# Performance work log

Hardware: AMD Instinct MI355X
Metric: run time of the kernel (lower is better)

Reference implementation:

```python
import jax, jax.numpy as jnp
import numpy as np

IOU_THRESH = 0.6
IMG_SIZE = 2048.0


def _iou_matrix(boxes):
    # boxes: [N, 4] as (x1, y1, x2, y2)
    x1, y1, x2, y2 = boxes[:, 0], boxes[:, 1], boxes[:, 2], boxes[:, 3]
    area = jnp.maximum(x2 - x1, 0.0) * jnp.maximum(y2 - y1, 0.0)  # [N]
    ix1 = jnp.maximum(x1[:, None], x1[None, :])
    iy1 = jnp.maximum(y1[:, None], y1[None, :])
    ix2 = jnp.minimum(x2[:, None], x2[None, :])
    iy2 = jnp.minimum(y2[:, None], y2[None, :])
    inter = jnp.maximum(ix2 - ix1, 0.0) * jnp.maximum(iy2 - iy1, 0.0)  # [N, N]
    union = area[:, None] + area[None, :] - inter
    return inter / jnp.maximum(union, 1e-9)


def _nms_keep(boxes, thresh):
    # Greedy NMS in the given (score-sorted) order; returns a [N] bool keep mask.
    n = boxes.shape[0]
    iou = _iou_matrix(boxes)  # [N, N] -- dominant memory traffic
    idx = jnp.arange(n)

    def step(suppressed, i):
        keep_i = jnp.logical_not(suppressed[i])
        # a kept box suppresses all LATER boxes with IoU > thresh
        suppressed = suppressed | (keep_i & (idx > i) & (iou[i] > thresh))
        return suppressed, keep_i

    _, keep = jax.lax.scan(step, jnp.zeros((n,), dtype=bool), idx)
    return keep


def _make_boxes(kc, ks, n):
    c = jax.random.uniform(kc, (n, 2), minval=0.0, maxval=IMG_SIZE)
    s = jax.random.uniform(ks, (n, 2), minval=10.0, maxval=120.0)
    return jnp.concatenate([c - s / 2, c + s / 2], axis=1)  # [n, 4]


def setup_inputs() -> dict:
    key = jax.random.key(0)
    k1, k2, k3, k4, k5, k6 = jax.random.split(key, 6)
    N = 8192  # vstacked detections across projections
    M = 8192  # vstacked RPN rois across projections
    det_boxes = _make_boxes(k1, k2, N)
    cls_scores = jax.random.normal(k3, (N, 4), dtype=jnp.float32)  # 4 TL classes, class 0 = invalid
    proj_id = jnp.zeros((N, 1), dtype=jnp.float32)
    detections = jnp.concatenate([proj_id, det_boxes, cls_scores], axis=1)  # [N, 9]
    rpn_boxes = _make_boxes(k4, k5, M)
    objness = jax.random.uniform(k6, (M, 1), dtype=jnp.float32)
    rpn_data = jnp.concatenate([jnp.zeros((M, 1), dtype=jnp.float32), rpn_boxes, objness], axis=1)  # [M, 6]
    return {"detections": detections, "rpn_data": rpn_data}


def reference(detections, rpn_data):
    # detect(): NMS(0.6) on detections[:, 1:5] and on rpn_data[:, 1:5]
    keep_det = _nms_keep(detections[:, 1:5], IOU_THRESH)  # [N] bool
    keep_rpn = _nms_keep(rpn_data[:, 1:5], IOU_THRESH)    # [M] bool
    # forward(): split surviving detections into valid (tl_type != 0) / invalid
    tl_types = jnp.argmax(detections[:, 5:], axis=1)
    valid_mask = keep_det & (tl_types != 0)
    invalid_mask = keep_det & (tl_types == 0)
    # fixed-shape (jit-friendly) masked outputs instead of data-dependent gather
    valid_detections = detections * valid_mask[:, None].astype(detections.dtype)
    invalid_detections = detections * invalid_mask[:, None].astype(detections.dtype)
    rpn_attack_data = rpn_data * keep_rpn[:, None].astype(rpn_data.dtype)
    return valid_detections, invalid_detections, rpn_attack_data
```

## Files before the change

### kernel.cpp

```cpp
#include <hip/hip_runtime.h>


constexpr int NROWS = 8192;
constexpr int NKW   = 256;
constexpr unsigned BCAP = 1536;
constexpr unsigned ACAP = 512;
constexpr unsigned RCAP = 2048;
constexpr unsigned ELDS = 16384;
#define IOU_T 0.6f

constexpr size_t OFF_EDGES = 4096;

__global__ __launch_bounds__(512) void scanpair_kernel(
    const float* __restrict__ det, const float* __restrict__ rpn,
    unsigned* __restrict__ cnts, unsigned* __restrict__ edges)
{
  const int cellid = blockIdx.x, set = blockIdx.y;
  const float* src  = (set == 0) ? det : rpn;
  const int    strd = (set == 0) ? 9 : 6;
  unsigned* myedges = edges + ((size_t)(set * 256 + cellid)) * RCAP;
  const int cx = cellid & 15, cy = cellid >> 4;

  __shared__ float Bx1[BCAP], By1[BCAP], Bx2[BCAP], By2[BCAP], Bar[BCAP];
  __shared__ unsigned Bid[BCAP];
  __shared__ unsigned aList[ACAP];
  __shared__ unsigned bCnt, aCnt, eCnt, ovf;

  const int t = threadIdx.x;
  if (t == 0) { bCnt = 0u; aCnt = 0u; eCnt = 0u; ovf = 0u; }
  __syncthreads();

  #pragma unroll
  for (int base = 0; base < 16; base += 8) {
    float rx1[8], ry1[8], rx2[8], ry2[8];
    #pragma unroll
    for (int k = 0; k < 8; ++k) {
      const int r = t + (base + k) * 512;
      const float* p = src + (size_t)r * strd + 1;
      rx1[k] = p[0]; ry1[k] = p[1]; rx2[k] = p[2]; ry2[k] = p[3];
    }
    #pragma unroll
    for (int k = 0; k < 8; ++k) {
      const int r = t + (base + k) * 512;
      const float x1 = rx1[k], y1 = ry1[k], x2 = rx2[k], y2 = ry2[k];
      const float cxe = 0.5f * (x1 + x2), cye = 0.5f * (y1 + y2);
      const int ccx = min(15, max(0, (int)(cxe * (1.0f / 128.0f))));
      const int ccy = min(15, max(0, (int)(cye * (1.0f / 128.0f))));
      const int dx = ccx - cx, dy = ccy - cy;
      if (dx >= -1 && dx <= 1 && dy >= -1 && dy <= 1) {
        const unsigned s = atomicAdd(&bCnt, 1u);
        if (s < BCAP) {
          Bx1[s] = x1; By1[s] = y1; Bx2[s] = x2; By2[s] = y2;
          Bar[s] = fmaxf(x2 - x1, 0.0f) * fmaxf(y2 - y1, 0.0f);
          Bid[s] = (unsigned)r;
          if (dx == 0 && dy == 0) {
            const unsigned as = atomicAdd(&aCnt, 1u);
            if (as < ACAP) aList[as] = s; else atomicOr(&ovf, 1u);
          }
        } else atomicOr(&ovf, 1u);
      }
    }
  }
  __syncthreads();

  const unsigned nb = min(bCnt, BCAP);
  const unsigned na = min(aCnt, ACAP);

  if (!ovf) {
    const unsigned tot = na * nb;
    for (unsigned p = t; p < tot; p += 512) {
      const unsigned ai = p / nb, x = p - ai * nb;
      const unsigned s = aList[ai];
      const unsigned ia = Bid[s], ib = Bid[x];
      if (ia < ib) {
        const float ix1 = fmaxf(Bx1[s], Bx1[x]), iy1 = fmaxf(By1[s], By1[x]);
        const float ix2 = fminf(Bx2[s], Bx2[x]), iy2 = fminf(By2[s], By2[x]);
        const float inter = fmaxf(ix2 - ix1, 0.0f) * fmaxf(iy2 - iy1, 0.0f);
        if (inter > 0.0f) {
          const float uni = Bar[s] + Bar[x] - inter;
          const float iou = inter / fmaxf(uni, 1e-9f);
          if (iou > IOU_T) {
            const unsigned slot = atomicAdd(&eCnt, 1u);
            if (slot < RCAP) myedges[slot] = (ia << 13) | ib;
          }
        }
      }
    }
  } else {
    for (int ra = 0; ra < NROWS; ++ra) {
      const float* pa = src + (size_t)ra * strd + 1;
      const float ax1 = pa[0], ay1 = pa[1], ax2 = pa[2], ay2 = pa[3];
      const float cxe = 0.5f * (ax1 + ax2), cye = 0.5f * (ay1 + ay2);
      const int ccx = min(15, max(0, (int)(cxe * (1.0f / 128.0f))));
      const int ccy = min(15, max(0, (int)(cye * (1.0f / 128.0f))));
      if (ccx != cx || ccy != cy) continue;
      const float aar = fmaxf(ax2 - ax1, 0.0f) * fmaxf(ay2 - ay1, 0.0f);
      for (int rb = t; rb < NROWS; rb += 512) {
        if ((unsigned)ra >= (unsigned)rb) continue;
        const float* pb = src + (size_t)rb * strd + 1;
        const float bx1 = pb[0], by1 = pb[1], bx2 = pb[2], by2 = pb[3];
        const float ix1 = fmaxf(ax1, bx1), iy1 = fmaxf(ay1, by1);
        const float ix2 = fminf(ax2, bx2), iy2 = fminf(ay2, by2);
        const float inter = fmaxf(ix2 - ix1, 0.0f) * fmaxf(iy2 - iy1, 0.0f);
        if (inter > 0.0f) {
          const float bar = fmaxf(bx2 - bx1, 0.0f) * fmaxf(by2 - by1, 0.0f);
          const float uni = aar + bar - inter;
          const float iou = inter / fmaxf(uni, 1e-9f);
          if (iou > IOU_T) {
            const unsigned slot = atomicAdd(&eCnt, 1u);
            if (slot < RCAP) myedges[slot] = ((unsigned)ra << 13) | (unsigned)rb;
          }
        }
      }
    }
  }
  __syncthreads();
  if (t == 0) cnts[set * 256 + cellid] = min(eCnt, RCAP);
}

__global__ __launch_bounds__(1024) void solve_epi_kernel(
    const float* __restrict__ det, const float* __restrict__ rpn,
    const unsigned* __restrict__ cnts, const unsigned* __restrict__ edges,
    float* __restrict__ out)
{
  const int blk = blockIdx.x;
  const int set = blk >> 4;
  const int slice = blk & 15;
  const unsigned* gedges = edges + (size_t)set * 256 * RCAP;

  __shared__ unsigned eL[ELDS];
  __shared__ unsigned rcnt[256], roff[256];
  __shared__ unsigned kbuf[2][NKW];
  __shared__ int changed[2];
  __shared__ unsigned Etot_sh;

  const int t = threadIdx.x;
  if (t < 256) rcnt[t] = min(cnts[set * 256 + t], RCAP);
  __syncthreads();

  if (t < 64) {
    const unsigned h0 = rcnt[4 * t], h1 = rcnt[4 * t + 1];
    const unsigned h2 = rcnt[4 * t + 2], h3 = rcnt[4 * t + 3];
    const unsigned lsum = h0 + h1 + h2 + h3;
    unsigned incl = lsum;
    #pragma unroll
    for (int d = 1; d < 64; d <<= 1) {
      const unsigned v = __shfl_up(incl, d);
      if (t >= d) incl += v;
    }
    const unsigned base = incl - lsum;
    roff[4 * t] = base;               roff[4 * t + 1] = base + h0;
    roff[4 * t + 2] = base + h0 + h1; roff[4 * t + 3] = base + h0 + h1 + h2;
    if (t == 63) Etot_sh = incl;
  }
  if (t < NKW) kbuf[0][t] = 0xFFFFFFFFu;
  __syncthreads();

  const unsigned Etot = Etot_sh;
  const bool cached = (Etot <= ELDS);
  if (cached) {
    const unsigned rg = (unsigned)t >> 2, ln = (unsigned)t & 3u;
    const unsigned c = rcnt[rg], o = roff[rg];
    for (unsigned k = ln; k < c; k += 4u)
      eL[o + k] = gedges[(size_t)rg * RCAP + k];
  }
  __syncthreads();

  int cur = 0;
  for (int round = 0; round < NROWS + 8; ++round) {
    const int nxt = cur ^ 1;
    if (t == 0) changed[round & 1] = 0;
    if (t < NKW) kbuf[nxt][t] = 0xFFFFFFFFu;
    __syncthreads();

    if (cached) {
      for (unsigned e = t; e < Etot; e += 1024) {
        const unsigned pk = eL[e];
        const unsigned i = pk >> 13, j = pk & 8191u;
        if ((kbuf[cur][i >> 5] >> (i & 31)) & 1u)
          atomicAnd(&kbuf[nxt][j >> 5], ~(1u << (j & 31)));
      }
    } else {
      for (unsigned r = (unsigned)t >> 2; r < 256u; r += 256u) {
        const unsigned c = rcnt[r];
        for (unsigned k = (unsigned)t & 3u; k < c; k += 4u) {
          const unsigned pk = gedges[(size_t)r * RCAP + k];
          const unsigned i = pk >> 13, j = pk & 8191u;
          if ((kbuf[cur][i >> 5] >> (i & 31)) & 1u)
            atomicAnd(&kbuf[nxt][j >> 5], ~(1u << (j & 31)));
        }
      }
    }
    __syncthreads();

    if (t < NKW && kbuf[nxt][t] != kbuf[cur][t]) changed[round & 1] = 1;
    __syncthreads();

    cur = nxt;
    if (!changed[round & 1]) break;
  }

  const int r0 = slice * 512;
  if (set == 0) {
    for (int i = r0 + t; i < r0 + 512; i += 1024) {
      const bool kd = (kbuf[cur][i >> 5] >> (i & 31)) & 1u;
      const float* p = det + (size_t)i * 9;
      const float sc0 = p[5], sc1 = p[6], sc2 = p[7], sc3 = p[8];
      int am = 0; float best = sc0;
      if (sc1 > best) { best = sc1; am = 1; }
      if (sc2 > best) { best = sc2; am = 2; }
      if (sc3 > best) { best = sc3; am = 3; }
      const float vm = (kd && am != 0) ? 1.0f : 0.0f;
      const float im = (kd && am == 0) ? 1.0f : 0.0f;
      float* o0 = out + (size_t)i * 9;
      float* o1 = out + (size_t)NROWS * 9 + (size_t)i * 9;
      #pragma unroll
      for (int c = 0; c < 9; ++c) { const float v = p[c]; o0[c] = v * vm; o1[c] = v * im; }
    }
  } else {
    for (int i = r0 + t; i < r0 + 512; i += 1024) {
      const bool kr = (kbuf[cur][i >> 5] >> (i & 31)) & 1u;
      const float rm = kr ? 1.0f : 0.0f;
      const float* q = rpn + (size_t)i * 6;
      float* o2 = out + (size_t)NROWS * 18 + (size_t)i * 6;
      #pragma unroll
      for (int c = 0; c < 6; ++c) o2[c] = q[c] * rm;
    }
  }
}

extern "C" void kernel_launch(void* const* d_in, const int* in_sizes, int n_in,
                              void* d_out, int out_size, void* d_ws, size_t ws_size,
                              hipStream_t stream)
{
  const float* det = (const float*)d_in[0];
  const float* rpn = (const float*)d_in[1];
  float* out = (float*)d_out;

  char* ws = (char*)d_ws;
  unsigned* cnts  = (unsigned*)ws;
  unsigned* edges = (unsigned*)(ws + OFF_EDGES);

  dim3 g1(256, 2);
  scanpair_kernel<<<g1, 512, 0, stream>>>(det, rpn, cnts, edges);
  solve_epi_kernel<<<32, 1024, 0, stream>>>(det, rpn, cnts, edges, out);
}
```

Baseline: 75.47 us.

## Replace per-cell pair blocks with per-row strip blocks using counting-sort binning

The pair-finding kernel now uses one block per grid row (16×2 blocks) instead of one per cell (256×2). Each block counting-sorts the boxes from its three neighbouring rows into column bins, then loops over the 16 cells in that row and tests each cell's boxes against its 3×3 neighbourhood. This cuts the number of blocks that each read all 8192 boxes, so far less redundant global load and binning work is done. The cost is a second input pass, a serial loop over columns inside each block, and only 32 blocks to fill the GPU. The solve kernel's edge-list bookkeeping shrinks to 16 rows per set to match.

```diff
diff --git a/kernel.cpp b/kernel.cpp
--- a/kernel.cpp
+++ b/kernel.cpp
@@ -3,33 +3,36 @@
 
 constexpr int NROWS = 8192;
 constexpr int NKW   = 256;
-constexpr unsigned BCAP = 1536;
-constexpr unsigned ACAP = 512;
-constexpr unsigned RCAP = 2048;
+constexpr unsigned SCAP = 2048;
+constexpr unsigned MCAP = 768;
+constexpr unsigned RCAP = 4096;
 constexpr unsigned ELDS = 16384;
 #define IOU_T 0.6f
 
 constexpr size_t OFF_EDGES = 4096;
 
-__global__ __launch_bounds__(512) void scanpair_kernel(
+__global__ __launch_bounds__(512) void strip_kernel(
     const float* __restrict__ det, const float* __restrict__ rpn,
     unsigned* __restrict__ cnts, unsigned* __restrict__ edges)
 {
-  const int cellid = blockIdx.x, set = blockIdx.y;
+  const int cy = blockIdx.x, set = blockIdx.y;
   const float* src  = (set == 0) ? det : rpn;
   const int    strd = (set == 0) ? 9 : 6;
-  unsigned* myedges = edges + ((size_t)(set * 256 + cellid)) * RCAP;
-  const int cx = cellid & 15, cy = cellid >> 4;
-
-  __shared__ float Bx1[BCAP], By1[BCAP], Bx2[BCAP], By2[BCAP], Bar[BCAP];
-  __shared__ unsigned Bid[BCAP];
-  __shared__ unsigned aList[ACAP];
-  __shared__ unsigned bCnt, aCnt, eCnt, ovf;
+  unsigned* myedges = edges + (size_t)(set * 16 + cy) * RCAP;
+
+  __shared__ float Sx1[SCAP], Sy1[SCAP], Sx2[SCAP], Sy2[SCAP], Sar[SCAP];
+  __shared__ unsigned Sid[SCAP];
+  __shared__ unsigned mlist[MCAP];
+  __shared__ unsigned shist[16], scur[16], soff[17];
+  __shared__ unsigned mhist[16], mcur[16], moff[17];
+  __shared__ unsigned eCnt, ovf;
 
   const int t = threadIdx.x;
-  if (t == 0) { bCnt = 0u; aCnt = 0u; eCnt = 0u; ovf = 0u; }
-  __syncthreads();
-
+  if (t < 16) { shist[t] = 0u; mhist[t] = 0u; scur[t] = 0u; mcur[t] = 0u; }
+  if (t == 0) { eCnt = 0u; ovf = 0u; }
+  __syncthreads();
+
+  int rcls[16];
   #pragma unroll
   for (int base = 0; base < 16; base += 8) {
     float rx1[8], ry1[8], rx2[8], ry2[8];
@@ -41,21 +44,59 @@
     }
     #pragma unroll
     for (int k = 0; k < 8; ++k) {
-      const int r = t + (base + k) * 512;
       const float x1 = rx1[k], y1 = ry1[k], x2 = rx2[k], y2 = ry2[k];
       const float cxe = 0.5f * (x1 + x2), cye = 0.5f * (y1 + y2);
       const int ccx = min(15, max(0, (int)(cxe * (1.0f / 128.0f))));
       const int ccy = min(15, max(0, (int)(cye * (1.0f / 128.0f))));
-      const int dx = ccx - cx, dy = ccy - cy;
-      if (dx >= -1 && dx <= 1 && dy >= -1 && dy <= 1) {
-        const unsigned s = atomicAdd(&bCnt, 1u);
-        if (s < BCAP) {
-          Bx1[s] = x1; By1[s] = y1; Bx2[s] = x2; By2[s] = y2;
-          Bar[s] = fmaxf(x2 - x1, 0.0f) * fmaxf(y2 - y1, 0.0f);
-          Bid[s] = (unsigned)r;
-          if (dx == 0 && dy == 0) {
-            const unsigned as = atomicAdd(&aCnt, 1u);
-            if (as < ACAP) aList[as] = s; else atomicOr(&ovf, 1u);
+      int cls = -1;
+      if (ccy >= cy - 1 && ccy <= cy + 1) {
+        cls = ccx | ((ccy == cy) ? 256 : 0);
+        atomicAdd(&shist[ccx], 1u);
+        if (ccy == cy) atomicAdd(&mhist[ccx], 1u);
+      }
+      rcls[base + k] = cls;
+    }
+  }
+  __syncthreads();
+
+  if (t < 64) {
+    const unsigned sv = (t < 16) ? shist[t] : 0u;
+    const unsigned mv = (t < 16) ? mhist[t] : 0u;
+    unsigned si = sv, mi = mv;
+    #pragma unroll
+    for (int d = 1; d < 16; d <<= 1) {
+      const unsigned a = __shfl_up(si, d);
+      const unsigned b = __shfl_up(mi, d);
+      if (t >= d) { si += a; mi += b; }
+    }
+    if (t < 16) { soff[t] = si - sv; moff[t] = mi - mv; }
+    if (t == 15) { soff[16] = si; moff[16] = mi; }
+  }
+  __syncthreads();
+
+  #pragma unroll
+  for (int base = 0; base < 16; base += 8) {
+    float rx1[8], ry1[8], rx2[8], ry2[8];
+    #pragma unroll
+    for (int k = 0; k < 8; ++k) {
+      const int r = t + (base + k) * 512;
+      const float* p = src + (size_t)r * strd + 1;
+      rx1[k] = p[0]; ry1[k] = p[1]; rx2[k] = p[2]; ry2[k] = p[3];
+    }
+    #pragma unroll
+    for (int k = 0; k < 8; ++k) {
+      const int cls = rcls[base + k];
+      if (cls >= 0) {
+        const int ccx = cls & 15;
+        const unsigned pos = soff[ccx] + atomicAdd(&scur[ccx], 1u);
+        if (pos < SCAP) {
+          const float x1 = rx1[k], y1 = ry1[k], x2 = rx2[k], y2 = ry2[k];
+          Sx1[pos] = x1; Sy1[pos] = y1; Sx2[pos] = x2; Sy2[pos] = y2;
+          Sar[pos] = fmaxf(x2 - x1, 0.0f) * fmaxf(y2 - y1, 0.0f);
+          Sid[pos] = (unsigned)(t + (base + k) * 512);
+          if (cls & 256) {
+            const unsigned mp = moff[ccx] + atomicAdd(&mcur[ccx], 1u);
+            if (mp < MCAP) mlist[mp] = pos; else atomicOr(&ovf, 1u);
           }
         } else atomicOr(&ovf, 1u);
       }
@@ -63,25 +104,36 @@
   }
   __syncthreads();
 
-  const unsigned nb = min(bCnt, BCAP);
-  const unsigned na = min(aCnt, ACAP);
-
   if (!ovf) {
-    const unsigned tot = na * nb;
-    for (unsigned p = t; p < tot; p += 512) {
-      const unsigned ai = p / nb, x = p - ai * nb;
-      const unsigned s = aList[ai];
-      const unsigned ia = Bid[s], ib = Bid[x];
-      if (ia < ib) {
-        const float ix1 = fmaxf(Bx1[s], Bx1[x]), iy1 = fmaxf(By1[s], By1[x]);
-        const float ix2 = fminf(Bx2[s], Bx2[x]), iy2 = fminf(By2[s], By2[x]);
-        const float inter = fmaxf(ix2 - ix1, 0.0f) * fmaxf(iy2 - iy1, 0.0f);
-        if (inter > 0.0f) {
-          const float uni = Bar[s] + Bar[x] - inter;
-          const float iou = inter / fmaxf(uni, 1e-9f);
-          if (iou > IOU_T) {
-            const unsigned slot = atomicAdd(&eCnt, 1u);
-            if (slot < RCAP) myedges[slot] = (ia << 13) | ib;
+    for (int cx = 0; cx < 16; ++cx) {
+      const unsigned nm = mhist[cx];
+      if (!nm) continue;
+      const unsigned mb = moff[cx];
+      const int xlo = (cx > 0) ? cx - 1 : 0;
+      const int xhi = (cx < 15) ? cx + 1 : 15;
+      const unsigned lo = soff[xlo], hi = soff[xhi + 1];
+      const unsigned nn = hi - lo;
+      if (!nn) continue;
+      const unsigned sh = (nn > 1) ? (32u - (unsigned)__builtin_clz(nn - 1)) : 0u;
+      const unsigned msk = (1u << sh) - 1u;
+      const unsigned tot = nm << sh;
+      for (unsigned p = t; p < tot; p += 512) {
+        const unsigned ni = p & msk;
+        if (ni >= nn) continue;
+        const unsigned m = mlist[mb + (p >> sh)];
+        const unsigned n = lo + ni;
+        const unsigned ia = Sid[m], ib = Sid[n];
+        if (ia < ib) {
+          const float ix1 = fmaxf(Sx1[m], Sx1[n]), iy1 = fmaxf(Sy1[m], Sy1[n]);
+          const float ix2 = fminf(Sx2[m], Sx2[n]), iy2 = fminf(Sy2[m], Sy2[n]);
+          const float inter = fmaxf(ix2 - ix1, 0.0f) * fmaxf(iy2 - iy1, 0.0f);
+          if (inter > 0.0f) {
+            const float uni = Sar[m] + Sar[n] - inter;
+            const float iou = inter / fmaxf(uni, 1e-9f);
+            if (iou > IOU_T) {
+              const unsigned slot = atomicAdd(&eCnt, 1u);
+              if (slot < RCAP) myedges[slot] = (ia << 13) | ib;
+            }
           }
         }
       }
@@ -90,10 +142,9 @@
     for (int ra = 0; ra < NROWS; ++ra) {
       const float* pa = src + (size_t)ra * strd + 1;
       const float ax1 = pa[0], ay1 = pa[1], ax2 = pa[2], ay2 = pa[3];
-      const float cxe = 0.5f * (ax1 + ax2), cye = 0.5f * (ay1 + ay2);
-      const int ccx = min(15, max(0, (int)(cxe * (1.0f / 128.0f))));
+      const float cye = 0.5f * (ay1 + ay2);
       const int ccy = min(15, max(0, (int)(cye * (1.0f / 128.0f))));
-      if (ccx != cx || ccy != cy) continue;
+      if (ccy != cy) continue;
       const float aar = fmaxf(ax2 - ax1, 0.0f) * fmaxf(ay2 - ay1, 0.0f);
       for (int rb = t; rb < NROWS; rb += 512) {
         if ((unsigned)ra >= (unsigned)rb) continue;
@@ -115,7 +166,7 @@
     }
   }
   __syncthreads();
-  if (t == 0) cnts[set * 256 + cellid] = min(eCnt, RCAP);
+  if (t == 0) cnts[set * 16 + cy] = min(eCnt, RCAP);
 }
 
 __global__ __launch_bounds__(1024) void solve_epi_kernel(
@@ -126,42 +177,37 @@
   const int blk = blockIdx.x;
   const int set = blk >> 4;
   const int slice = blk & 15;
-  const unsigned* gedges = edges + (size_t)set * 256 * RCAP;
+  const unsigned* gedges = edges + (size_t)set * 16 * RCAP;
 
   __shared__ unsigned eL[ELDS];
-  __shared__ unsigned rcnt[256], roff[256];
+  __shared__ unsigned rcnt[16], roff[17];
   __shared__ unsigned kbuf[2][NKW];
   __shared__ int changed[2];
-  __shared__ unsigned Etot_sh;
 
   const int t = threadIdx.x;
-  if (t < 256) rcnt[t] = min(cnts[set * 256 + t], RCAP);
+  if (t < 16) rcnt[t] = min(cnts[set * 16 + t], RCAP);
   __syncthreads();
 
   if (t < 64) {
-    const unsigned h0 = rcnt[4 * t], h1 = rcnt[4 * t + 1];
-    const unsigned h2 = rcnt[4 * t + 2], h3 = rcnt[4 * t + 3];
-    const unsigned lsum = h0 + h1 + h2 + h3;
-    unsigned incl = lsum;
-    #pragma unroll
-    for (int d = 1; d < 64; d <<= 1) {
-      const unsigned v = __shfl_up(incl, d);
-      if (t >= d) incl += v;
-    }
-    const unsigned base = incl - lsum;
-    roff[4 * t] = base;               roff[4 * t + 1] = base + h0;
-    roff[4 * t + 2] = base + h0 + h1; roff[4 * t + 3] = base + h0 + h1 + h2;
-    if (t == 63) Etot_sh = incl;
+    const unsigned v = (t < 16) ? rcnt[t] : 0u;
+    unsigned incl = v;
+    #pragma unroll
+    for (int d = 1; d < 16; d <<= 1) {
+      const unsigned a = __shfl_up(incl, d);
+      if (t >= d) incl += a;
+    }
+    if (t < 16) roff[t] = incl - v;
+    if (t == 15) roff[16] = incl;
   }
   if (t < NKW) kbuf[0][t] = 0xFFFFFFFFu;
   __syncthreads();
 
-  const unsigned Etot = Etot_sh;
+  const unsigned Etot = roff[16];
   const bool cached = (Etot <= ELDS);
   if (cached) {
-    const unsigned rg = (unsigned)t >> 2, ln = (unsigned)t & 3u;
+    const unsigned rg = (unsigned)t >> 6, ln = (unsigned)t & 63u;
     const unsigned c = rcnt[rg], o = roff[rg];
-    for (unsigned k = ln; k < c; k += 4u)
+    for (unsigned k = ln; k < c; k += 64u)
       eL[o + k] = gedges[(size_t)rg * RCAP + k];
   }
   __syncthreads();
@@ -181,14 +227,13 @@
           atomicAnd(&kbuf[nxt][j >> 5], ~(1u << (j & 31)));
       }
     } else {
-      for (unsigned r = (unsigned)t >> 2; r < 256u; r += 256u) {
-        const unsigned c = rcnt[r];
-        for (unsigned k = (unsigned)t & 3u; k < c; k += 4u) {
-          const unsigned pk = gedges[(size_t)r * RCAP + k];
-          const unsigned i = pk >> 13, j = pk & 8191u;
-          if ((kbuf[cur][i >> 5] >> (i & 31)) & 1u)
-            atomicAnd(&kbuf[nxt][j >> 5], ~(1u << (j & 31)));
-        }
+      const unsigned rg = (unsigned)t >> 6, ln = (unsigned)t & 63u;
+      const unsigned c = rcnt[rg];
+      for (unsigned k = ln; k < c; k += 64u) {
+        const unsigned pk = gedges[(size_t)rg * RCAP + k];
+        const unsigned i = pk >> 13, j = pk & 8191u;
+        if ((kbuf[cur][i >> 5] >> (i & 31)) & 1u)
+          atomicAnd(&kbuf[nxt][j >> 5], ~(1u << (j & 31)));
       }
     }
     __syncthreads();
@@ -241,7 +286,7 @@
   unsigned* cnts  = (unsigned*)ws;
   unsigned* edges = (unsigned*)(ws + OFF_EDGES);
 
-  dim3 g1(256, 2);
-  scanpair_kernel<<<g1, 512, 0, stream>>>(det, rpn, cnts, edges);
+  dim3 g1(16, 2);
+  strip_kernel<<<g1, 512, 0, stream>>>(det, rpn, cnts, edges);
   solve_epi_kernel<<<32, 1024, 0, stream>>>(det, rpn, cnts, edges, out);
 }
```

After: 202.2 us. +167.9%, slower.
